# Kernel tuning notes

Hardware: AMD Instinct MI355X
Metric: run time of the kernel (lower is better)

## Reference

```python
import jax, jax.numpy as jnp
import numpy as np

D = 1024
H = 16
HD = D // H
FF = 4 * D
LN_EPS = 1e-5


def _layernorm(x, w, b):
    mu = jnp.mean(x, axis=-1, keepdims=True)
    var = jnp.mean(jnp.square(x - mu), axis=-1, keepdims=True)
    return (x - mu) * jax.lax.rsqrt(var + LN_EPS) * w + b


def setup_inputs() -> dict:
    key = jax.random.key(0)
    ks = jax.random.split(key, 12)
    s = 0.02
    return {
        "x": jax.random.normal(ks[0], (8, 1024, D), jnp.float32),
        "c": jax.random.normal(ks[1], (8, D), jnp.float32),
        "ln1_w": jnp.ones((D,), jnp.float32),
        "ln1_b": jnp.zeros((D,), jnp.float32),
        "ln2_w": jnp.ones((D,), jnp.float32),
        "ln2_b": jnp.zeros((D,), jnp.float32),
        "ada_w": jax.random.normal(ks[2], (D, 6 * D), jnp.float32) * s,
        "ada_b": jnp.zeros((6 * D,), jnp.float32),
        "qkv_w": jax.random.normal(ks[3], (D, 3 * D), jnp.float32) * s,
        "qkv_b": jnp.zeros((3 * D,), jnp.float32),
        "proj_w": jax.random.normal(ks[4], (D, D), jnp.float32) * s,
        "proj_b": jnp.zeros((D,), jnp.float32),
        "fc1_w": jax.random.normal(ks[5], (D, FF), jnp.float32) * s,
        "fc1_b": jnp.zeros((FF,), jnp.float32),
        "fc2_w": jax.random.normal(ks[6], (FF, D), jnp.float32) * s,
        "fc2_b": jnp.zeros((D,), jnp.float32),
    }


def reference(x, c, ln1_w, ln1_b, ln2_w, ln2_b, ada_w, ada_b,
              qkv_w, qkv_b, proj_w, proj_b, fc1_w, fc1_b, fc2_w, fc2_b):
    B, L, _ = x.shape
    # adaLN modulation: SiLU(c) @ W -> 6 chunks of (B, D)
    ssg = jax.nn.silu(c) @ ada_w + ada_b
    msa_shift, msa_scale, msa_gate, mlp_shift, mlp_scale, mlp_gate = jnp.split(ssg, 6, axis=-1)

    def modulate(h, shift, scale):
        return h * (1.0 + scale[:, None, :]) + shift[:, None, :]

    # ---- attention branch ----
    h = modulate(_layernorm(x, ln1_w, ln1_b), msa_shift, msa_scale)
    qkv = h @ qkv_w + qkv_b                      # (B, L, 3D)
    q, k, v = jnp.split(qkv, 3, axis=-1)
    q = q.reshape(B, L, H, HD).transpose(0, 2, 1, 3)   # (B, H, L, HD)
    k = k.reshape(B, L, H, HD).transpose(0, 2, 1, 3)
    v = v.reshape(B, L, H, HD).transpose(0, 2, 1, 3)
    scores = jnp.einsum("bhqd,bhkd->bhqk", q, k) / jnp.sqrt(jnp.float32(HD))
    attn = jax.nn.softmax(scores, axis=-1)
    a = jnp.einsum("bhqk,bhkd->bhqd", attn, v)   # (B, H, L, HD)
    a = a.transpose(0, 2, 1, 3).reshape(B, L, D)
    a = a @ proj_w + proj_b
    x = x + msa_gate[:, None, :] * a

    # ---- MLP branch ----
    h = modulate(_layernorm(x, ln2_w, ln2_b), mlp_shift, mlp_scale)
    h = jax.nn.gelu(h @ fc1_w + fc1_b, approximate=True)
    h = h @ fc2_w + fc2_b
    x = x + mlp_gate[:, None, :] * h
    return x
```

## Files before the change

kernel.cpp:

```cpp
#include <hip/hip_runtime.h>
#include <math.h>

#define DMODEL 1024
#define SIXD   6144
#define NHEAD  16
#define HEADD  64
#define LSEQ   1024
#define NBATCH 8
#define MROWS  8192

typedef unsigned short ushort_t;
typedef __attribute__((ext_vector_type(8))) short bf16x8;
typedef __attribute__((ext_vector_type(4))) float f32x4;

__device__ __forceinline__ unsigned short f2bf(float f) {
  unsigned int u = __float_as_uint(f);
  u += 0x7fff + ((u >> 16) & 1);
  return (unsigned short)(u >> 16);
}

__device__ __forceinline__ void gload_lds16(const void* g, void* l) {
  __builtin_amdgcn_global_load_lds(
      (const __attribute__((address_space(1))) unsigned int*)g,
      (__attribute__((address_space(3))) unsigned int*)l, 16, 0, 0);
}

__global__ void tcast_kernel(const float* __restrict__ W, ushort_t* __restrict__ WT,
                             int K, int N) {
  __shared__ float tile[32][33];
  int tx = threadIdx.x & 31, ty = threadIdx.x >> 5;
  int n0 = blockIdx.x * 32, k0 = blockIdx.y * 32;
#pragma unroll
  for (int r = 0; r < 4; ++r)
    tile[ty + 8*r][tx] = W[(size_t)(k0 + ty + 8*r) * N + n0 + tx];
  __syncthreads();
#pragma unroll
  for (int r = 0; r < 4; ++r)
    WT[(size_t)(n0 + ty + 8*r) * K + k0 + tx] = f2bf(tile[tx][ty + 8*r]);
}

__global__ void ada_kernel(const float* __restrict__ c, const float* __restrict__ ada_w,
                           const float* __restrict__ ada_b, float* __restrict__ ssg) {
  __shared__ float s[DMODEL];
  int b = blockIdx.y;
  int j = blockIdx.x * 256 + threadIdx.x;
  for (int i = threadIdx.x; i < DMODEL; i += 256) {
    float v = c[b * DMODEL + i];
    s[i] = v / (1.0f + __expf(-v));
  }
  __syncthreads();
  float acc = ada_b[j];
#pragma unroll 8
  for (int k = 0; k < DMODEL; ++k)
    acc = fmaf(s[k], ada_w[(size_t)k * SIXD + j], acc);
  ssg[b * SIXD + j] = acc;
}

__global__ __launch_bounds__(256) void ln_mod_kernel(
    const float* __restrict__ xin, const float* __restrict__ lw,
    const float* __restrict__ lb, const float* __restrict__ ssg,
    int shift_off, int scale_off, ushort_t* __restrict__ outB) {
  int row = blockIdx.x;
  int b = row >> 10;
  int tid = threadIdx.x;
  float4 v = ((const float4*)xin)[(size_t)row * 256 + tid];
  float sum = v.x + v.y + v.z + v.w;
  float sq  = v.x*v.x + v.y*v.y + v.z*v.z + v.w*v.w;
#pragma unroll
  for (int m = 32; m; m >>= 1) { sum += __shfl_xor(sum, m); sq += __shfl_xor(sq, m); }
  __shared__ float rbuf[8];
  int w = tid >> 6, lane = tid & 63;
  if (lane == 0) { rbuf[w] = sum; rbuf[4 + w] = sq; }
  __syncthreads();
  sum = rbuf[0] + rbuf[1] + rbuf[2] + rbuf[3];
  sq  = rbuf[4] + rbuf[5] + rbuf[6] + rbuf[7];
  float mu  = sum * (1.0f / 1024.0f);
  float var = sq * (1.0f / 1024.0f) - mu * mu;
  float rs  = rsqrtf(var + 1e-5f);
  const float* sg = ssg + b * SIXD;
  float vv[4] = {v.x, v.y, v.z, v.w};
  ushort4 pk;
  unsigned short* pks = (unsigned short*)&pk;
#pragma unroll
  for (int j = 0; j < 4; ++j) {
    int d = tid * 4 + j;
    float h = (vv[j] - mu) * rs * lw[d] + lb[d];
    h = h * (1.0f + sg[scale_off + d]) + sg[shift_off + d];
    pks[j] = f2bf(h);
  }
  ((ushort4*)outB)[(size_t)row * 256 + tid] = pk;
}

template <int EPI>
__global__ __launch_bounds__(256, 2) void gemm_kernel(
    const ushort_t* __restrict__ A, const ushort_t* __restrict__ BT,
    const float* __restrict__ bias, const float* __restrict__ ssg,
    const float* resid, float* outF, ushort_t* __restrict__ outB,
    int N, int K, int gate_off) {
  __shared__ __align__(16) char As[16384];
  __shared__ __align__(16) char Bs[16384];
  int tid = threadIdx.x, lane = tid & 63, w = tid >> 6;
  int l15 = lane & 15, g = lane >> 4;
  int m0 = blockIdx.y * 128, n0 = blockIdx.x * 128;
  int wrow = (w >> 1) * 64, wcol = (w & 1) * 64;
  f32x4 zero = {0.f, 0.f, 0.f, 0.f};
  f32x4 acc[4][4];
#pragma unroll
  for (int i = 0; i < 4; ++i)
#pragma unroll
    for (int j = 0; j < 4; ++j) acc[i][j] = zero;

  for (int k0 = 0; k0 < K; k0 += 64) {
#pragma unroll
    for (int p = 0; p < 4; ++p) {
      int flat = p * 4096 + w * 1024 + lane * 16;
      int row = flat >> 7;
      int colb = (flat & 127) ^ ((row & 7) << 4);
      gload_lds16((const char*)A  + ((size_t)(m0 + row) * K + k0) * 2 + colb,
                  As + p * 4096 + w * 1024);
      gload_lds16((const char*)BT + ((size_t)(n0 + row) * K + k0) * 2 + colb,
                  Bs + p * 4096 + w * 1024);
    }
    __syncthreads();
#pragma unroll
    for (int kk = 0; kk < 2; ++kk) {
      bf16x8 af[4], bfr[4];
#pragma unroll
      for (int i = 0; i < 4; ++i) {
        int ar = wrow + i * 16 + l15;
        af[i]  = *(const bf16x8*)(As + ar * 128 + ((kk * 64 + g * 16) ^ ((ar & 7) << 4)));
        int br = wcol + i * 16 + l15;
        bfr[i] = *(const bf16x8*)(Bs + br * 128 + ((kk * 64 + g * 16) ^ ((br & 7) << 4)));
      }
#pragma unroll
      for (int i = 0; i < 4; ++i)
#pragma unroll
        for (int j = 0; j < 4; ++j)
          acc[i][j] = __builtin_amdgcn_mfma_f32_16x16x32_bf16(af[i], bfr[j], acc[i][j], 0, 0, 0);
    }
    __syncthreads();
  }
#pragma unroll
  for (int i = 0; i < 4; ++i)
#pragma unroll
    for (int j = 0; j < 4; ++j)
#pragma unroll
      for (int r = 0; r < 4; ++r) {
        int grow = m0 + wrow + i * 16 + g * 4 + r;
        int gcol = n0 + wcol + j * 16 + l15;
        float v = acc[i][j][r] + bias[gcol];
        if (EPI == 0) {
          outB[(size_t)grow * N + gcol] = f2bf(v);
        } else if (EPI == 1 || EPI == 3) {
          int bb = grow >> 10;
          float gate = ssg[bb * SIXD + gate_off + gcol];
          size_t idx = (size_t)grow * N + gcol;
          outF[idx] = resid[idx] + gate * v;
        } else {
          float u = v;
          float t = 0.7978845608028654f * (u + 0.044715f * u * u * u);
          float e = __expf(2.0f * t);
          float th = 1.0f - 2.0f / (e + 1.0f);
          outB[(size_t)grow * N + gcol] = f2bf(0.5f * u * (1.0f + th));
        }
      }
}

__global__ __launch_bounds__(256, 2) void attn_kernel(
    const ushort_t* __restrict__ qkv,
    ushort_t* __restrict__ aout) {
  __shared__ __align__(16) char Ksm[8192];
  __shared__ __align__(16) char Vsm[8192];
  __shared__ __align__(16) char Psm[8192];
  int tid = threadIdx.x, lane = tid & 63, w = tid >> 6;
  int l15 = lane & 15, g = lane >> 4;
  int qt = blockIdx.x;
  int bh = blockIdx.y;
  int b = bh >> 4, h = bh & 15;

  bf16x8 aq[2];
  {
    int qrow = qt * 64 + w * 16 + l15;
    const short* qp = (const short*)qkv + (size_t)(b * LSEQ + qrow) * 3072 + h * 64 + g * 8;
    aq[0] = *(const bf16x8*)qp;
    aq[1] = *(const bf16x8*)(qp + 32);
  }
  f32x4 zero = {0.f, 0.f, 0.f, 0.f};
  f32x4 o[4] = {zero, zero, zero, zero};
  float mrow[4] = {-INFINITY, -INFINITY, -INFINITY, -INFINITY};
  float lrow[4] = {0.f, 0.f, 0.f, 0.f};
  const float scale = 0.125f;

  for (int t = 0; t < 16; ++t) {
    int kv0 = t * 64;
#pragma unroll
    for (int p = 0; p < 2; ++p) {
      int flat = p * 4096 + w * 1024 + lane * 16;
      int row = flat >> 7;
      int colb = (flat & 127) ^ ((row & 7) << 4);
      const char* src = (const char*)qkv +
          ((size_t)(b * LSEQ + kv0 + row) * 3072 + 1024 + h * 64) * 2 + colb;
      gload_lds16(src, Ksm + p * 4096 + w * 1024);
    }
#pragma unroll
    for (int i = 0; i < 2; ++i) {
      int flat = tid + 256 * i;
      int kv = flat >> 3, dc = flat & 7;
      const short* vp = (const short*)qkv +
          (size_t)(b * LSEQ + kv0 + kv) * 3072 + 2048 + h * 64 + dc * 8;
      bf16x8 vv = *(const bf16x8*)vp;
#pragma unroll
      for (int j = 0; j < 8; ++j) {
        int d = dc * 8 + j;
        *(short*)(Vsm + d * 128 + ((kv * 2) ^ ((d & 7) << 4))) = vv[j];
      }
    }
    __syncthreads();
    f32x4 s[4] = {zero, zero, zero, zero};
#pragma unroll
    for (int c = 0; c < 4; ++c)
#pragma unroll
      for (int kk = 0; kk < 2; ++kk) {
        int key = c * 16 + l15;
        bf16x8 bk = *(const bf16x8*)(Ksm + key * 128 + ((kk * 64 + g * 16) ^ ((key & 7) << 4)));
        s[c] = __builtin_amdgcn_mfma_f32_16x16x32_bf16(aq[kk], bk, s[c], 0, 0, 0);
      }
    float pf[4][4];
#pragma unroll
    for (int r = 0; r < 4; ++r) {
      float mx = -INFINITY;
#pragma unroll
      for (int c = 0; c < 4; ++c) { s[c][r] *= scale; mx = fmaxf(mx, s[c][r]); }
      mx = fmaxf(mx, __shfl_xor(mx, 1)); mx = fmaxf(mx, __shfl_xor(mx, 2));
      mx = fmaxf(mx, __shfl_xor(mx, 4)); mx = fmaxf(mx, __shfl_xor(mx, 8));
      float mnew = fmaxf(mrow[r], mx);
      float alpha = __expf(mrow[r] - mnew);
      float sump = 0.f;
#pragma unroll
      for (int c = 0; c < 4; ++c) {
        float p = __expf(s[c][r] - mnew);
        pf[c][r] = p; sump += p;
      }
      sump += __shfl_xor(sump, 1); sump += __shfl_xor(sump, 2);
      sump += __shfl_xor(sump, 4); sump += __shfl_xor(sump, 8);
      lrow[r] = lrow[r] * alpha + sump;
      mrow[r] = mnew;
#pragma unroll
      for (int n = 0; n < 4; ++n) o[n][r] *= alpha;
    }
    char* pb = Psm + w * 2048;
#pragma unroll
    for (int c = 0; c < 4; ++c)
#pragma unroll
      for (int r = 0; r < 4; ++r) {
        int row = g * 4 + r;
        int colb = (c * 16 + l15) * 2;
        *(short*)(pb + row * 128 + (colb ^ ((row & 7) << 4))) = (short)f2bf(pf[c][r]);
      }
#pragma unroll
    for (int kk = 0; kk < 2; ++kk) {
      bf16x8 ap = *(const bf16x8*)(pb + l15 * 128 + ((kk * 64 + g * 16) ^ ((l15 & 7) << 4)));
#pragma unroll
      for (int n = 0; n < 4; ++n) {
        int d = n * 16 + l15;
        bf16x8 bv = *(const bf16x8*)(Vsm + d * 128 + ((kk * 64 + g * 16) ^ ((d & 7) << 4)));
        o[n] = __builtin_amdgcn_mfma_f32_16x16x32_bf16(ap, bv, o[n], 0, 0, 0);
      }
    }
    __syncthreads();
  }
#pragma unroll
  for (int r = 0; r < 4; ++r) {
    float rl = 1.0f / lrow[r];
    int qrow = qt * 64 + w * 16 + g * 4 + r;
#pragma unroll
    for (int n = 0; n < 4; ++n) {
      int d = h * 64 + n * 16 + l15;
      aout[(size_t)(b * LSEQ + qrow) * 1024 + d] = f2bf(o[n][r] * rl);
    }
  }
}

extern "C" void kernel_launch(void* const* d_in, const int* in_sizes, int n_in,
                              void* d_out, int out_size, void* d_ws, size_t ws_size,
                              hipStream_t stream) {
  const float* x      = (const float*)d_in[0];
  const float* c      = (const float*)d_in[1];
  const float* ln1_w  = (const float*)d_in[2];
  const float* ln1_b  = (const float*)d_in[3];
  const float* ln2_w  = (const float*)d_in[4];
  const float* ln2_b  = (const float*)d_in[5];
  const float* ada_w  = (const float*)d_in[6];
  const float* ada_b  = (const float*)d_in[7];
  const float* qkv_w  = (const float*)d_in[8];
  const float* qkv_b  = (const float*)d_in[9];
  const float* proj_w = (const float*)d_in[10];
  const float* proj_b = (const float*)d_in[11];
  const float* fc1_w  = (const float*)d_in[12];
  const float* fc1_b  = (const float*)d_in[13];
  const float* fc2_w  = (const float*)d_in[14];
  const float* fc2_b  = (const float*)d_in[15];
  float* out = (float*)d_out;
  char* ws = (char*)d_ws;

  ushort_t* qkvT  = (ushort_t*)(ws + 0);
  ushort_t* projT = (ushort_t*)(ws + 6291456);
  ushort_t* fc1T  = (ushort_t*)(ws + 8388608);
  ushort_t* fc2T  = (ushort_t*)(ws + 16777216);
  float*    ssg   = (float*)(ws + 25165824);
  ushort_t* hbuf  = (ushort_t*)(ws + 25362432);
  ushort_t* abuf  = hbuf;
  ushort_t* qkvb  = (ushort_t*)(ws + 42139648);
  if (ws_size < (size_t)109248512) return;

  tcast_kernel<<<dim3(96, 32),  256, 0, stream>>>(qkv_w,  qkvT, 1024, 3072);
  tcast_kernel<<<dim3(32, 32),  256, 0, stream>>>(proj_w, projT, 1024, 1024);
  tcast_kernel<<<dim3(128, 32), 256, 0, stream>>>(fc1_w,  fc1T, 1024, 4096);
  tcast_kernel<<<dim3(32, 128), 256, 0, stream>>>(fc2_w,  fc2T, 4096, 1024);
  ada_kernel<<<dim3(24, 8), 256, 0, stream>>>(c, ada_w, ada_b, ssg);

  ln_mod_kernel<<<8192, 256, 0, stream>>>(x, ln1_w, ln1_b, ssg, 0, 1024, hbuf);
  gemm_kernel<0><<<dim3(24, 64), 256, 0, stream>>>(hbuf, qkvT, qkv_b, nullptr,
                                                   nullptr, nullptr, qkvb, 3072, 1024, 0);
  attn_kernel<<<dim3(16, 128), 256, 0, stream>>>(qkvb, abuf);
  gemm_kernel<1><<<dim3(8, 64), 256, 0, stream>>>(abuf, projT, proj_b, ssg,
                                                  x, out, nullptr, 1024, 1024, 2048);
  ln_mod_kernel<<<8192, 256, 0, stream>>>(out, ln2_w, ln2_b, ssg, 3072, 4096, hbuf);
  gemm_kernel<2><<<dim3(32, 64), 256, 0, stream>>>(hbuf, fc1T, fc1_b, nullptr,
                                                   nullptr, nullptr, qkvb, 4096, 1024, 0);
  gemm_kernel<3><<<dim3(8, 64), 256, 0, stream>>>(qkvb, fc2T, fc2_b, ssg,
                                                  out, out, nullptr, 1024, 4096, 5120);
}
```

Measured before the change: 505.3 us.

## Double-buffer K/V tiles and keep P in registers in attention kernel

Restructures the flash-attention loop so K and V for the next tile are fetched into a second LDS buffer while the current tile is computed, cutting one barrier per iteration. It also swaps the QK MFMA operands so each lane holds a full query row, uses exp2 with a pre-folded log2e scale, and skips the rescale of the output accumulators when the running max does not change. P is packed to bf16 with a cvt_pk instruction and redistributed through lane shuffles instead of an LDS round trip. The costs are more LDS per block, more shuffles, and a small LDS buffer used to broadcast alpha and the final normaliser.

```diff
diff --git a/kernel.cpp b/kernel.cpp
--- a/kernel.cpp
+++ b/kernel.cpp
@@ -169,13 +169,11 @@
 __global__ __launch_bounds__(256, 2) void attn_kernel(
     const ushort_t* __restrict__ qkv,
     ushort_t* __restrict__ aout) {
-  __shared__ __align__(16) char Ksm[8192];
-  __shared__ __align__(16) char Vsm[8192];
-  __shared__ __align__(16) char Psm[8192];
+  __shared__ __align__(16) char SM[33024];
+  float* alphab = (float*)(SM + 32768);
   int tid = threadIdx.x, lane = tid & 63, w = tid >> 6;
   int l15 = lane & 15, g = lane >> 4;
-  int qt = blockIdx.x;
-  int bh = blockIdx.y;
+  int qt = blockIdx.x, bh = blockIdx.y;
   int b = bh >> 4, h = bh & 15;
 
   bf16x8 aq[2];
@@ -185,100 +183,156 @@
     aq[0] = *(const bf16x8*)qp;
     aq[1] = *(const bf16x8*)(qp + 32);
   }
+
+  const char* ksrc[2];
+#pragma unroll
+  for (int p = 0; p < 2; ++p) {
+    int flat = p * 4096 + w * 1024 + lane * 16;
+    int row = flat >> 7;
+    int colb = (flat & 127) ^ ((row & 7) << 4);
+    ksrc[p] = (const char*)qkv + ((size_t)(b * LSEQ + row) * 3072 + 1024 + h * 64) * 2 + colb;
+  }
+  const short* vsrc[2];
+  int vkv[2], vdc[2];
+#pragma unroll
+  for (int i = 0; i < 2; ++i) {
+    int flat = tid + 256 * i;
+    vkv[i] = flat >> 3;
+    vdc[i] = flat & 7;
+    vsrc[i] = (const short*)qkv + (size_t)(b * LSEQ + vkv[i]) * 3072 + 2048 + h * 64 + vdc[i] * 8;
+  }
+
   f32x4 zero = {0.f, 0.f, 0.f, 0.f};
   f32x4 o[4] = {zero, zero, zero, zero};
-  float mrow[4] = {-INFINITY, -INFINITY, -INFINITY, -INFINITY};
-  float lrow[4] = {0.f, 0.f, 0.f, 0.f};
-  const float scale = 0.125f;
+  float mrow = -INFINITY;
+  float lrow = 0.f;
+  const float sc = 0.18033688f;
+
+#pragma unroll
+  for (int p = 0; p < 2; ++p) gload_lds16(ksrc[p], SM + p * 4096 + w * 1024);
+#pragma unroll
+  for (int i = 0; i < 2; ++i) {
+    bf16x8 vv = *(const bf16x8*)vsrc[i];
+    char* vb = SM + 16384;
+#pragma unroll
+    for (int j = 0; j < 8; ++j) {
+      int d = vdc[i] * 8 + j;
+      *(short*)(vb + d * 128 + ((vkv[i] * 2) ^ ((d & 7) << 4))) = vv[j];
+    }
+  }
+  __syncthreads();
 
   for (int t = 0; t < 16; ++t) {
-    int kv0 = t * 64;
-#pragma unroll
-    for (int p = 0; p < 2; ++p) {
-      int flat = p * 4096 + w * 1024 + lane * 16;
-      int row = flat >> 7;
-      int colb = (flat & 127) ^ ((row & 7) << 4);
-      const char* src = (const char*)qkv +
-          ((size_t)(b * LSEQ + kv0 + row) * 3072 + 1024 + h * 64) * 2 + colb;
-      gload_lds16(src, Ksm + p * 4096 + w * 1024);
-    }
-#pragma unroll
-    for (int i = 0; i < 2; ++i) {
-      int flat = tid + 256 * i;
-      int kv = flat >> 3, dc = flat & 7;
-      const short* vp = (const short*)qkv +
-          (size_t)(b * LSEQ + kv0 + kv) * 3072 + 2048 + h * 64 + dc * 8;
-      bf16x8 vv = *(const bf16x8*)vp;
-#pragma unroll
-      for (int j = 0; j < 8; ++j) {
-        int d = dc * 8 + j;
-        *(short*)(Vsm + d * 128 + ((kv * 2) ^ ((d & 7) << 4))) = vv[j];
-      }
-    }
+    int cur = t & 1;
+    bf16x8 vn[2];
+    if (t < 15) {
+      size_t koff = (size_t)(t + 1) * (64 * 3072 * 2);
+#pragma unroll
+      for (int p = 0; p < 2; ++p)
+        gload_lds16(ksrc[p] + koff, SM + (cur ^ 1) * 8192 + p * 4096 + w * 1024);
+#pragma unroll
+      for (int i = 0; i < 2; ++i)
+        vn[i] = *(const bf16x8*)(vsrc[i] + (size_t)(t + 1) * (64 * 3072));
+    }
+    f32x4 s4[4] = {zero, zero, zero, zero};
+#pragma unroll
+    for (int c = 0; c < 4; ++c)
+#pragma unroll
+      for (int ks = 0; ks < 2; ++ks) {
+        int key = c * 16 + l15;
+        bf16x8 ak = *(const bf16x8*)(SM + cur * 8192 + key * 128 +
+                                     ((ks * 64 + g * 16) ^ ((key & 7) << 4)));
+        s4[c] = __builtin_amdgcn_mfma_f32_16x16x32_bf16(ak, aq[ks], s4[c], 0, 0, 0);
+      }
+    float z[16], mx = -INFINITY;
+#pragma unroll
+    for (int c = 0; c < 4; ++c)
+#pragma unroll
+      for (int r = 0; r < 4; ++r) {
+        float t2 = s4[c][r] * sc;
+        z[c * 4 + r] = t2;
+        mx = fmaxf(mx, t2);
+      }
+    mx = fmaxf(mx, __shfl_xor(mx, 16));
+    mx = fmaxf(mx, __shfl_xor(mx, 32));
+    bool need = __any(mx > mrow);
+    if (need) {
+      float mnew = fmaxf(mrow, mx);
+      float alpha = exp2f(mrow - mnew);
+      mrow = mnew;
+      if (lane < 16) alphab[w * 16 + lane] = alpha;
+      lrow *= alpha;
+    }
+    float p16[16], sump = 0.f;
+#pragma unroll
+    for (int i = 0; i < 16; ++i) {
+      float p = exp2f(z[i] - mrow);
+      p16[i] = p;
+      sump += p;
+    }
+    sump += __shfl_xor(sump, 16);
+    sump += __shfl_xor(sump, 32);
+    lrow += sump;
+    if (need) {
+      f32x4 av = *(const f32x4*)&alphab[w * 16 + g * 4];
+#pragma unroll
+      for (int nb = 0; nb < 4; ++nb)
+#pragma unroll
+        for (int r = 0; r < 4; ++r) o[nb][r] *= av[r];
+    }
+    unsigned pk[8];
+#pragma unroll
+    for (int c = 0; c < 4; ++c)
+#pragma unroll
+      for (int m = 0; m < 2; ++m)
+        asm("v_cvt_pk_bf16_f32 %0, %1, %2"
+            : "=v"(pk[c * 2 + m]) : "v"(p16[c * 4 + 2 * m]), "v"(p16[c * 4 + 2 * m + 1]));
+    unsigned pa[2][4];
+    int gl = (g & 1) * 2;
+#pragma unroll
+    for (int kb = 0; kb < 2; ++kb)
+#pragma unroll
+      for (int wv = 0; wv < 4; ++wv) {
+        int srcl = l15 + (gl + (wv >> 1)) * 16;
+        unsigned vA = (unsigned)__shfl((int)pk[kb * 4 + (wv & 1)], srcl);
+        unsigned vB = (unsigned)__shfl((int)pk[kb * 4 + 2 + (wv & 1)], srcl);
+        pa[kb][wv] = (g >> 1) ? vB : vA;
+      }
+    if (t < 15) {
+      char* vb = SM + 16384 + (cur ^ 1) * 8192;
+#pragma unroll
+      for (int i = 0; i < 2; ++i)
+#pragma unroll
+        for (int j = 0; j < 8; ++j) {
+          int d = vdc[i] * 8 + j;
+          *(short*)(vb + d * 128 + ((vkv[i] * 2) ^ ((d & 7) << 4))) = vn[i][j];
+        }
+    }
+    union PU { unsigned u[4]; bf16x8 v; };
+    PU pu0, pu1;
+#pragma unroll
+    for (int i = 0; i < 4; ++i) { pu0.u[i] = pa[0][i]; pu1.u[i] = pa[1][i]; }
+#pragma unroll
+    for (int kb = 0; kb < 2; ++kb)
+#pragma unroll
+      for (int nb = 0; nb < 4; ++nb) {
+        int d = nb * 16 + l15;
+        bf16x8 bv = *(const bf16x8*)(SM + 16384 + cur * 8192 + d * 128 +
+                                     ((kb * 64 + g * 16) ^ ((d & 7) << 4)));
+        o[nb] = __builtin_amdgcn_mfma_f32_16x16x32_bf16(kb ? pu1.v : pu0.v, bv, o[nb], 0, 0, 0);
+      }
     __syncthreads();
-    f32x4 s[4] = {zero, zero, zero, zero};
-#pragma unroll
-    for (int c = 0; c < 4; ++c)
-#pragma unroll
-      for (int kk = 0; kk < 2; ++kk) {
-        int key = c * 16 + l15;
-        bf16x8 bk = *(const bf16x8*)(Ksm + key * 128 + ((kk * 64 + g * 16) ^ ((key & 7) << 4)));
-        s[c] = __builtin_amdgcn_mfma_f32_16x16x32_bf16(aq[kk], bk, s[c], 0, 0, 0);
-      }
-    float pf[4][4];
+  }
+  if (lane < 16) alphab[w * 16 + lane] = 1.0f / lrow;
+  f32x4 rl = *(const f32x4*)&alphab[w * 16 + g * 4];
+#pragma unroll
+  for (int nb = 0; nb < 4; ++nb)
 #pragma unroll
     for (int r = 0; r < 4; ++r) {
-      float mx = -INFINITY;
-#pragma unroll
-      for (int c = 0; c < 4; ++c) { s[c][r] *= scale; mx = fmaxf(mx, s[c][r]); }
-      mx = fmaxf(mx, __shfl_xor(mx, 1)); mx = fmaxf(mx, __shfl_xor(mx, 2));
-      mx = fmaxf(mx, __shfl_xor(mx, 4)); mx = fmaxf(mx, __shfl_xor(mx, 8));
-      float mnew = fmaxf(mrow[r], mx);
-      float alpha = __expf(mrow[r] - mnew);
-      float sump = 0.f;
-#pragma unroll
-      for (int c = 0; c < 4; ++c) {
-        float p = __expf(s[c][r] - mnew);
-        pf[c][r] = p; sump += p;
-      }
-      sump += __shfl_xor(sump, 1); sump += __shfl_xor(sump, 2);
-      sump += __shfl_xor(sump, 4); sump += __shfl_xor(sump, 8);
-      lrow[r] = lrow[r] * alpha + sump;
-      mrow[r] = mnew;
-#pragma unroll
-      for (int n = 0; n < 4; ++n) o[n][r] *= alpha;
-    }
-    char* pb = Psm + w * 2048;
-#pragma unroll
-    for (int c = 0; c < 4; ++c)
-#pragma unroll
-      for (int r = 0; r < 4; ++r) {
-        int row = g * 4 + r;
-        int colb = (c * 16 + l15) * 2;
-        *(short*)(pb + row * 128 + (colb ^ ((row & 7) << 4))) = (short)f2bf(pf[c][r]);
-      }
-#pragma unroll
-    for (int kk = 0; kk < 2; ++kk) {
-      bf16x8 ap = *(const bf16x8*)(pb + l15 * 128 + ((kk * 64 + g * 16) ^ ((l15 & 7) << 4)));
-#pragma unroll
-      for (int n = 0; n < 4; ++n) {
-        int d = n * 16 + l15;
-        bf16x8 bv = *(const bf16x8*)(Vsm + d * 128 + ((kk * 64 + g * 16) ^ ((d & 7) << 4)));
-        o[n] = __builtin_amdgcn_mfma_f32_16x16x32_bf16(ap, bv, o[n], 0, 0, 0);
-      }
-    }
-    __syncthreads();
-  }
-#pragma unroll
-  for (int r = 0; r < 4; ++r) {
-    float rl = 1.0f / lrow[r];
-    int qrow = qt * 64 + w * 16 + g * 4 + r;
-#pragma unroll
-    for (int n = 0; n < 4; ++n) {
-      int d = h * 64 + n * 16 + l15;
-      aout[(size_t)(b * LSEQ + qrow) * 1024 + d] = f2bf(o[n][r] * rl);
-    }
-  }
+      int qrow = qt * 64 + w * 16 + g * 4 + r;
+      aout[(size_t)(b * LSEQ + qrow) * 1024 + h * 64 + nb * 16 + l15] =
+          f2bf(o[nb][r] * rl[r]);
+    }
 }
 
 extern "C" void kernel_launch(void* const* d_in, const int* in_sizes, int n_in,
```

Measured after the change: 475.8 us. -5.8%, faster.
